# Kernel optimization log

Hardware: AMD Instinct MI355X
Metric: run time of the kernel (lower is better)

## Reference

```python
import jax, jax.numpy as jnp
import numpy as np
import math

D_MODEL = 1024
NUM_HEADS = 16
BATCH = 2
SEQ = 2048

def setup_inputs() -> dict:
    key = jax.random.key(0)
    ks = jax.random.split(key, 9)
    s = 1.0 / math.sqrt(D_MODEL)
    inp = {
        "X": jax.random.normal(ks[0], (BATCH, SEQ, D_MODEL), dtype=jnp.float32),
        "Wq": jax.random.uniform(ks[1], (D_MODEL, D_MODEL), jnp.float32, -s, s),
        "bq": jax.random.uniform(ks[2], (D_MODEL,), jnp.float32, -s, s),
        "Wk": jax.random.uniform(ks[3], (D_MODEL, D_MODEL), jnp.float32, -s, s),
        "bk": jax.random.uniform(ks[4], (D_MODEL,), jnp.float32, -s, s),
        "Wv": jax.random.uniform(ks[5], (D_MODEL, D_MODEL), jnp.float32, -s, s),
        "bv": jax.random.uniform(ks[6], (D_MODEL,), jnp.float32, -s, s),
        "Wo": jax.random.uniform(ks[7], (D_MODEL, D_MODEL), jnp.float32, -s, s),
        "bo": jax.random.uniform(ks[8], (D_MODEL,), jnp.float32, -s, s),
    }
    return inp

def reference(X, Wq, bq, Wk, bk, Wv, bv, Wo, bo):
    B, S, D = X.shape
    H = NUM_HEADS
    dk = D // H
    # QKV projections (Linear: x @ W.T + b; here W stored as [in, out] so x @ W + b)
    q = X @ Wq + bq
    k = X @ Wk + bk
    v = X @ Wv + bv
    # split heads -> [B, H, S, dk]
    q = q.reshape(B, S, H, dk).transpose(0, 2, 1, 3)
    k = k.reshape(B, S, H, dk).transpose(0, 2, 1, 3)
    v = v.reshape(B, S, H, dk).transpose(0, 2, 1, 3)
    scores = jnp.einsum("bhqd,bhkd->bhqk", q, k) / math.sqrt(dk)
    weights = jax.nn.softmax(scores, axis=-1)
    attn = jnp.einsum("bhqk,bhkd->bhqd", weights, v)
    concat = attn.transpose(0, 2, 1, 3).reshape(B, S, D)
    return concat @ Wo + bo
```

## Files before the change

kernel.cpp:

```cpp
#include <hip/hip_runtime.h>
#include <stdint.h>

#define D_MODEL 1024
#define NH      16
#define DKH     64
#define BATCH   2
#define SEQ     2048
#define M_TOK   (BATCH*SEQ)

typedef __attribute__((ext_vector_type(8))) short bf16x8;
typedef __attribute__((ext_vector_type(4))) float f32x4;

__device__ __forceinline__ uint16_t f2b(float f) {
  uint32_t u = __builtin_bit_cast(uint32_t, f);
  return (uint16_t)((u + 0x7FFFu + ((u >> 16) & 1u)) >> 16);
}

__device__ __forceinline__ void gl2lds16(const uint16_t* g, uint16_t* l) {
  __builtin_amdgcn_global_load_lds(
      (const __attribute__((address_space(1))) void*)g,
      (__attribute__((address_space(3))) void*)l, 16, 0, 0);
}

__global__ void convx(const float* __restrict__ X, uint16_t* __restrict__ Xb) {
  int i = (blockIdx.x * 256 + threadIdx.x) * 8;
  float4 a = *(const float4*)(X + i);
  float4 b = *(const float4*)(X + i + 4);
  uint16_t tmp[8] = {f2b(a.x), f2b(a.y), f2b(a.z), f2b(a.w),
                     f2b(b.x), f2b(b.y), f2b(b.z), f2b(b.w)};
  *(uint4*)(Xb + i) = *(const uint4*)tmp;
}

__global__ void wtrans(const float* __restrict__ W0, const float* __restrict__ W1,
                       const float* __restrict__ W2, const float* __restrict__ W3,
                       uint16_t* __restrict__ T0, uint16_t* __restrict__ T1,
                       uint16_t* __restrict__ T2, uint16_t* __restrict__ T3) {
  __shared__ float tile[32][33];
  int z = blockIdx.z;
  const float* W = (z == 0) ? W0 : (z == 1) ? W1 : (z == 2) ? W2 : W3;
  uint16_t*    T = (z == 0) ? T0 : (z == 1) ? T1 : (z == 2) ? T2 : T3;
  int k0 = blockIdx.x * 32, n0 = blockIdx.y * 32;
  int tx = threadIdx.x, ty = threadIdx.y;
  tile[ty][tx] = W[(size_t)(k0 + ty) * D_MODEL + n0 + tx];
  __syncthreads();
  T[(size_t)(n0 + ty) * D_MODEL + k0 + tx] = f2b(tile[tx][ty]);
}

template <bool SWAP>
__device__ __forceinline__ void gemm_core(const uint16_t* __restrict__ A,
                                          const uint16_t* __restrict__ BT,
                                          uint16_t* As, uint16_t* Bs,
                                          int m0, int n0, int kBeg, int kEnd,
                                          f32x4 (&acc)[4][4]) {
  const int t    = threadIdx.x;
  const int lane = t & 63;
  const int qi   = lane & 15, g = lane >> 4;
  const int wm   = (t >> 7) & 1;
  const int wn   = (t >> 6) & 1;
  const int srow = t >> 2;
  const int sc   = (t & 3) ^ ((t >> 3) & 3);
  const int wbase = t & 192;
  const int rch  = (g ^ ((qi >> 1) & 3)) * 8;

  const uint16_t* Ag = A  + (size_t)(m0 + srow) * D_MODEL + sc * 8;
  const uint16_t* Bg = BT + (size_t)(n0 + srow) * D_MODEL + sc * 8;

#pragma unroll
  for (int j = 0; j < 2; j++) {
    gl2lds16(Ag + (size_t)j * 64 * D_MODEL + kBeg, As + (j * 256 + wbase) * 8);
    gl2lds16(Bg + (size_t)j * 64 * D_MODEL + kBeg, Bs + (j * 256 + wbase) * 8);
  }

  int cur = 0;
  for (int k0 = kBeg; k0 < kEnd; k0 += 32) {
    __syncthreads();
    int kn = k0 + 32;
    if (kn < kEnd) {
      int nb = (cur ^ 1) * 4096;
#pragma unroll
      for (int j = 0; j < 2; j++) {
        gl2lds16(Ag + (size_t)j * 64 * D_MODEL + kn, As + nb + (j * 256 + wbase) * 8);
        gl2lds16(Bg + (size_t)j * 64 * D_MODEL + kn, Bs + nb + (j * 256 + wbase) * 8);
      }
    }
    const uint16_t* Ab = As + cur * 4096;
    const uint16_t* Bb = Bs + cur * 4096;
    bf16x8 af[4], bf[4];
#pragma unroll
    for (int i = 0; i < 4; i++) {
      af[i] = *(const bf16x8*)(Ab + (wm * 64 + i * 16 + qi) * 32 + rch);
      bf[i] = *(const bf16x8*)(Bb + (wn * 64 + i * 16 + qi) * 32 + rch);
    }
#pragma unroll
    for (int i = 0; i < 4; i++)
#pragma unroll
      for (int j = 0; j < 4; j++)
        acc[i][j] = SWAP
          ? __builtin_amdgcn_mfma_f32_16x16x32_bf16(bf[j], af[i], acc[i][j], 0, 0, 0)
          : __builtin_amdgcn_mfma_f32_16x16x32_bf16(af[i], bf[j], acc[i][j], 0, 0, 0);
    cur ^= 1;
  }
}

__global__ __launch_bounds__(256) void qkv_gemm(
    const uint16_t* __restrict__ Xb,
    const uint16_t* __restrict__ WqT, const uint16_t* __restrict__ WkT,
    const uint16_t* __restrict__ WvT,
    const float* __restrict__ bq, const float* __restrict__ bk,
    const float* __restrict__ bv,
    uint16_t* __restrict__ Qo, uint16_t* __restrict__ Ko, uint16_t* __restrict__ Vt) {
  __shared__ __align__(16) uint16_t smem[17408];
  uint16_t* As = smem;
  uint16_t* Bs = smem + 8192;
  uint16_t* T  = smem;
  const int z = blockIdx.z;
  const uint16_t* BT  = (z == 0) ? WqT : (z == 1) ? WkT : WvT;
  const float*   bias = (z == 0) ? bq  : (z == 1) ? bk  : bv;
  const int m0 = blockIdx.y * 128, n0 = blockIdx.x * 128;
  const int lane = threadIdx.x & 63, qi = lane & 15, g = lane >> 4;
  const int wm = (threadIdx.x >> 7) & 1, wn = (threadIdx.x >> 6) & 1;
  const float l2e = 1.4426950408889634f * 0.125f;

  const f32x4 ZERO = {0.f, 0.f, 0.f, 0.f};
  f32x4 acc[4][4];
#pragma unroll
  for (int i = 0; i < 4; i++)
#pragma unroll
    for (int j = 0; j < 4; j++) acc[i][j] = ZERO;

  if (z == 2) {
    gemm_core<false>(Xb, BT, As, Bs, m0, n0, 0, D_MODEL, acc);
    __syncthreads();
#pragma unroll
    for (int i = 0; i < 4; i++) {
      int tok = wm * 64 + i * 16 + g * 4;
#pragma unroll
      for (int j = 0; j < 4; j++) {
        int ch = wn * 64 + j * 16 + qi;
        float bb = bias[n0 + ch];
        uint32_t lo = (uint32_t)f2b(acc[i][j][0] + bb) | ((uint32_t)f2b(acc[i][j][1] + bb) << 16);
        uint32_t hi = (uint32_t)f2b(acc[i][j][2] + bb) | ((uint32_t)f2b(acc[i][j][3] + bb) << 16);
        uint2 pk = {lo, hi};
        *(uint2*)(T + ch * 136 + tok) = pk;
      }
    }
    __syncthreads();
    {
      int ch = threadIdx.x >> 1, sh = threadIdx.x & 1;
      const uint16_t* src = T + ch * 136 + sh * 64;
      int bidx = m0 >> 11;
      uint16_t* dst = Vt + ((size_t)(bidx * D_MODEL + n0 + ch)) * SEQ + (m0 & 2047) + sh * 64;
#pragma unroll
      for (int u = 0; u < 8; u++)
        *(uint4*)(dst + u * 8) = *(const uint4*)(src + u * 8);
    }
  } else {
    gemm_core<true>(Xb, BT, As, Bs, m0, n0, 0, D_MODEL, acc);
    uint16_t* O = z ? Ko : Qo;
    const float osc = (z == 0) ? l2e : 1.0f;
#pragma unroll
    for (int i = 0; i < 4; i++) {
      size_t tok = m0 + wm * 64 + i * 16 + qi;
#pragma unroll
      for (int j = 0; j < 4; j++) {
        int ch = n0 + wn * 64 + j * 16 + g * 4;
        float4 bb = *(const float4*)(bias + ch);
        uint32_t lo = (uint32_t)f2b((acc[i][j][0] + bb.x) * osc) |
                      ((uint32_t)f2b((acc[i][j][1] + bb.y) * osc) << 16);
        uint32_t hi = (uint32_t)f2b((acc[i][j][2] + bb.z) * osc) |
                      ((uint32_t)f2b((acc[i][j][3] + bb.w) * osc) << 16);
        uint2 pk = {lo, hi};
        *(uint2*)(O + tok * D_MODEL + ch) = pk;
      }
    }
  }
}

__global__ __launch_bounds__(256) void oproj_gemm(
    const uint16_t* __restrict__ Ab, const uint16_t* __restrict__ WoT,
    const float* __restrict__ bo, float* __restrict__ out) {
  __shared__ __align__(16) uint16_t As[8192];
  __shared__ __align__(16) uint16_t Bs[4096];
  const int t = threadIdx.x;
  const int lane = t & 63, qi = lane & 15, g = lane >> 4;
  const int wm = (t >> 7) & 1;
  const int wn = (t >> 6) & 1;
  const int srow = t >> 2;
  const int sc = (t & 3) ^ ((t >> 3) & 3);
  const int wbase = t & 192;
  const int rch = (g ^ ((qi >> 1) & 3)) * 8;
  const int m0 = blockIdx.y * 128, n0 = blockIdx.x * 64;

  const uint16_t* Ag = Ab  + (size_t)(m0 + srow) * D_MODEL + sc * 8;
  const uint16_t* Bg = WoT + (size_t)(n0 + srow) * D_MODEL + sc * 8;

  const f32x4 ZERO = {0.f, 0.f, 0.f, 0.f};
  f32x4 acc[4][2];
#pragma unroll
  for (int i = 0; i < 4; i++)
#pragma unroll
    for (int j = 0; j < 2; j++) acc[i][j] = ZERO;

  gl2lds16(Ag, As + wbase * 8);
  gl2lds16(Ag + (size_t)64 * D_MODEL, As + (256 + wbase) * 8);
  gl2lds16(Bg, Bs + wbase * 8);

  int cur = 0;
  for (int k0 = 0; k0 < D_MODEL; k0 += 32) {
    __syncthreads();
    int kn = k0 + 32;
    if (kn < D_MODEL) {
      int nbA = (cur ^ 1) * 4096, nbB = (cur ^ 1) * 2048;
      gl2lds16(Ag + kn, As + nbA + wbase * 8);
      gl2lds16(Ag + (size_t)64 * D_MODEL + kn, As + nbA + (256 + wbase) * 8);
      gl2lds16(Bg + kn, Bs + nbB + wbase * 8);
    }
    const uint16_t* Abuf = As + cur * 4096;
    const uint16_t* Bbuf = Bs + cur * 2048;
    bf16x8 af[4], bf[2];
#pragma unroll
    for (int i = 0; i < 4; i++)
      af[i] = *(const bf16x8*)(Abuf + (wm * 64 + i * 16 + qi) * 32 + rch);
#pragma unroll
    for (int j = 0; j < 2; j++)
      bf[j] = *(const bf16x8*)(Bbuf + (wn * 32 + j * 16 + qi) * 32 + rch);
#pragma unroll
    for (int i = 0; i < 4; i++)
#pragma unroll
      for (int j = 0; j < 2; j++)
        acc[i][j] = __builtin_amdgcn_mfma_f32_16x16x32_bf16(bf[j], af[i], acc[i][j], 0, 0, 0);
    cur ^= 1;
  }

#pragma unroll
  for (int i = 0; i < 4; i++) {
    size_t tok = m0 + wm * 64 + i * 16 + qi;
#pragma unroll
    for (int j = 0; j < 2; j++) {
      int ch = n0 + wn * 32 + j * 16 + g * 4;
      float4 bb = *(const float4*)(bo + ch);
      float4 o = {acc[i][j][0] + bb.x, acc[i][j][1] + bb.y,
                  acc[i][j][2] + bb.z, acc[i][j][3] + bb.w};
      *(float4*)(out + tok * D_MODEL + ch) = o;
    }
  }
}

__global__ __launch_bounds__(256) void attn_fwd(
    const uint16_t* __restrict__ Q, const uint16_t* __restrict__ K,
    const uint16_t* __restrict__ Vt, uint16_t* __restrict__ O) {
  __shared__ __align__(16) uint16_t sm[24576];
  uint16_t* Ps = sm + 16384;

  const int t = threadIdx.x, lane = t & 63, w = t >> 6;
  const int g = lane >> 4, qi = lane & 15;
  const int wbase = t & 192;
  const int sc = (t & 3) ^ ((t >> 3) & 3);
  const int rch = (g ^ ((qi >> 1) & 3)) * 8;
  const int key = qi & 7;
  const int q0 = blockIdx.x * 128;
  const int bh = blockIdx.y, b = bh >> 4, h = bh & 15;
  const uint16_t* Qp = Q + (size_t)b * SEQ * D_MODEL + h * DKH;
  const uint16_t* Kp = K + (size_t)b * SEQ * D_MODEL + h * DKH;
  const uint16_t* Vp = Vt + (size_t)bh * DKH * SEQ;

  const int srow = t >> 2, c8 = sc * 8;

#pragma unroll
  for (int hs = 0; hs < 2; hs++)
#pragma unroll
    for (int j = 0; j < 2; j++)
      gl2lds16(Qp + (size_t)(q0 + j * 64 + srow) * D_MODEL + hs * 32 + c8,
               sm + 16384 + hs * 4096 + (j * 256 + wbase) * 8);
  {
    const uint16_t* Kr = Kp + (size_t)srow * D_MODEL;
    const uint16_t* Vr = Vp + (size_t)srow * SEQ;
    gl2lds16(Kr + c8,      sm + wbase * 8);
    gl2lds16(Kr + 32 + c8, sm + 2048 + wbase * 8);
    gl2lds16(Vr + c8,      sm + 8192 + wbase * 8);
    gl2lds16(Vr + 32 + c8, sm + 8192 + 2048 + wbase * 8);
  }
  __syncthreads();

  bf16x8 qf[2][2];
#pragma unroll
  for (int ks = 0; ks < 2; ks++)
#pragma unroll
    for (int i = 0; i < 2; i++)
      qf[ks][i] = *(const bf16x8*)(sm + 16384 + ks * 4096 + (w * 32 + i * 16 + qi) * 32 + rch);
  __syncthreads();

  float lsum[2] = {0.f, 0.f};
  const f32x4 ZERO = {0.f, 0.f, 0.f, 0.f};
  f32x4 oaccT[4][2];
#pragma unroll
  for (int d = 0; d < 4; d++)
#pragma unroll
    for (int i = 0; i < 2; i++) oaccT[d][i] = ZERO;

  int cur = 0;
  for (int kt = 0; kt < SEQ / 64; kt++) {
    if (kt + 1 < SEQ / 64) {
      int nb = (cur ^ 1) * 4096;
      const uint16_t* Kr = Kp + (size_t)((kt + 1) * 64 + srow) * D_MODEL;
      const uint16_t* Vr = Vp + (size_t)srow * SEQ + (kt + 1) * 64;
      gl2lds16(Kr + c8,      sm + nb + wbase * 8);
      gl2lds16(Kr + 32 + c8, sm + nb + 2048 + wbase * 8);
      gl2lds16(Vr + c8,      sm + 8192 + nb + wbase * 8);
      gl2lds16(Vr + 32 + c8, sm + 8192 + nb + 2048 + wbase * 8);
    }
    const uint16_t* Kb = sm + cur * 4096;
    const uint16_t* Vb = sm + 8192 + cur * 4096;

    f32x4 sacc[4][2];
#pragma unroll
    for (int j = 0; j < 4; j++)
#pragma unroll
      for (int i = 0; i < 2; i++) sacc[j][i] = ZERO;
#pragma unroll
    for (int ks = 0; ks < 2; ks++) {
      const uint16_t* Ksb = Kb + ks * 2048;
      bf16x8 kf[4];
#pragma unroll
      for (int j = 0; j < 4; j++)
        kf[j] = *(const bf16x8*)(Ksb + (j * 16 + qi) * 32 + rch);
#pragma unroll
      for (int j = 0; j < 4; j++)
#pragma unroll
        for (int i = 0; i < 2; i++)
          sacc[j][i] = __builtin_amdgcn_mfma_f32_16x16x32_bf16(kf[j], qf[ks][i], sacc[j][i], 0, 0, 0);
    }

#pragma unroll
    for (int i = 0; i < 2; i++) {
      uint16_t* Pr = Ps + (w * 32 + i * 16 + qi) * 64;
#pragma unroll
      for (int j = 0; j < 4; j++) {
        float p0 = __builtin_amdgcn_exp2f(sacc[j][i][0]);
        float p1 = __builtin_amdgcn_exp2f(sacc[j][i][1]);
        float p2 = __builtin_amdgcn_exp2f(sacc[j][i][2]);
        float p3 = __builtin_amdgcn_exp2f(sacc[j][i][3]);
        lsum[i] += (p0 + p1) + (p2 + p3);
        uint2 pk = {__builtin_amdgcn_perm(__builtin_bit_cast(uint32_t, p1),
                                          __builtin_bit_cast(uint32_t, p0), 0x07060302u),
                    __builtin_amdgcn_perm(__builtin_bit_cast(uint32_t, p3),
                                          __builtin_bit_cast(uint32_t, p2), 0x07060302u)};
        *(uint2*)(Pr + (((j * 4 + g) ^ (2 * key)) << 2)) = pk;
      }
    }

#pragma unroll
    for (int ks = 0; ks < 2; ks++) {
      const uint16_t* Vsb = Vb + ks * 2048;
      bf16x8 vf[4], pf[2];
#pragma unroll
      for (int d = 0; d < 4; d++)
        vf[d] = *(const bf16x8*)(Vsb + (d * 16 + qi) * 32 + rch);
#pragma unroll
      for (int i = 0; i < 2; i++)
        pf[i] = *(const bf16x8*)(Ps + (w * 32 + i * 16 + qi) * 64 +
                                 (((ks * 4 + g) ^ key) << 3));
#pragma unroll
      for (int d = 0; d < 4; d++)
#pragma unroll
        for (int i = 0; i < 2; i++)
          oaccT[d][i] = __builtin_amdgcn_mfma_f32_16x16x32_bf16(vf[d], pf[i], oaccT[d][i], 0, 0, 0);
    }

    if (kt + 1 < SEQ / 64) __syncthreads();
    cur ^= 1;
  }

#pragma unroll
  for (int i = 0; i < 2; i++) {
    lsum[i] += __shfl_xor(lsum[i], 16, 64);
    lsum[i] += __shfl_xor(lsum[i], 32, 64);
  }
  float rl[2] = {1.f / lsum[0], 1.f / lsum[1]};

#pragma unroll
  for (int i = 0; i < 2; i++) {
    size_t row = (size_t)b * SEQ + q0 + w * 32 + i * 16 + qi;
#pragma unroll
    for (int d = 0; d < 4; d++) {
      uint32_t lo = (uint32_t)f2b(oaccT[d][i][0] * rl[i]) |
                    ((uint32_t)f2b(oaccT[d][i][1] * rl[i]) << 16);
      uint32_t hi = (uint32_t)f2b(oaccT[d][i][2] * rl[i]) |
                    ((uint32_t)f2b(oaccT[d][i][3] * rl[i]) << 16);
      uint2 pk = {lo, hi};
      *(uint2*)(O + row * D_MODEL + h * DKH + d * 16 + g * 4) = pk;
    }
  }
}

extern "C" void kernel_launch(void* const* d_in, const int* in_sizes, int n_in,
                              void* d_out, int out_size, void* d_ws, size_t ws_size,
                              hipStream_t stream) {
  (void)in_sizes; (void)n_in; (void)out_size; (void)ws_size;
  const float* X  = (const float*)d_in[0];
  const float* Wq = (const float*)d_in[1];
  const float* bq = (const float*)d_in[2];
  const float* Wk = (const float*)d_in[3];
  const float* bk = (const float*)d_in[4];
  const float* Wv = (const float*)d_in[5];
  const float* bv = (const float*)d_in[6];
  const float* Wo = (const float*)d_in[7];
  const float* bo = (const float*)d_in[8];
  float* out = (float*)d_out;

  char* p = (char*)d_ws;
  uint16_t* Xb  = (uint16_t*)p; p += (size_t)M_TOK * D_MODEL * 2;
  uint16_t* WqT = (uint16_t*)p; p += (size_t)D_MODEL * D_MODEL * 2;
  uint16_t* WkT = (uint16_t*)p; p += (size_t)D_MODEL * D_MODEL * 2;
  uint16_t* WvT = (uint16_t*)p; p += (size_t)D_MODEL * D_MODEL * 2;
  uint16_t* WoT = (uint16_t*)p; p += (size_t)D_MODEL * D_MODEL * 2;
  uint16_t* Qw  = (uint16_t*)p; p += (size_t)M_TOK * D_MODEL * 2;
  uint16_t* Kw  = (uint16_t*)p; p += (size_t)M_TOK * D_MODEL * 2;
  uint16_t* Vt  = (uint16_t*)p; p += (size_t)M_TOK * D_MODEL * 2;
  uint16_t* Ob  = (uint16_t*)p; p += (size_t)M_TOK * D_MODEL * 2;

  convx<<<(M_TOK * D_MODEL) / (256 * 8), 256, 0, stream>>>(X, Xb);
  wtrans<<<dim3(32, 32, 4), dim3(32, 32), 0, stream>>>(Wq, Wk, Wv, Wo, WqT, WkT, WvT, WoT);
  qkv_gemm<<<dim3(8, 32, 3), 256, 0, stream>>>(Xb, WqT, WkT, WvT, bq, bk, bv, Qw, Kw, Vt);
  attn_fwd<<<dim3(SEQ / 128, BATCH * NH), 256, 0, stream>>>(Qw, Kw, Vt, Ob);
  oproj_gemm<<<dim3(16, 32), 256, 0, stream>>>(Ob, WoT, bo, out);
}
```

Baseline: 203.9 us.

## Split attention block across 8 waves with 16 query rows each

The attention kernel moves from 256 to 512 threads per block, so each wave handles 16 query rows instead of 32. Q fragments are now loaded straight from global memory into registers rather than staged through LDS, and the K/V tile loads are divided across the two 256-thread halves. s_setprio raises wave priority around the MFMA groups. The aim is more waves in flight to hide latency and lower per-wave register pressure. The cost is that each wave now issues K/V fragment LDS reads for half as many MFMAs, so LDS traffic per unit of compute doubles.

```diff
diff --git a/kernel.cpp b/kernel.cpp
--- a/kernel.cpp
+++ b/kernel.cpp
@@ -246,7 +246,7 @@
   }
 }
 
-__global__ __launch_bounds__(256) void attn_fwd(
+__global__ __launch_bounds__(512, 4) void attn_fwd(
     const uint16_t* __restrict__ Q, const uint16_t* __restrict__ K,
     const uint16_t* __restrict__ Vt, uint16_t* __restrict__ O) {
   __shared__ __align__(16) uint16_t sm[24576];
@@ -254,8 +254,6 @@
 
   const int t = threadIdx.x, lane = t & 63, w = t >> 6;
   const int g = lane >> 4, qi = lane & 15;
-  const int wbase = t & 192;
-  const int sc = (t & 3) ^ ((t >> 3) & 3);
   const int rch = (g ^ ((qi >> 1) & 3)) * 8;
   const int key = qi & 7;
   const int q0 = blockIdx.x * 128;
@@ -264,59 +262,45 @@
   const uint16_t* Kp = K + (size_t)b * SEQ * D_MODEL + h * DKH;
   const uint16_t* Vp = Vt + (size_t)bh * DKH * SEQ;
 
-  const int srow = t >> 2, c8 = sc * 8;
-
-#pragma unroll
-  for (int hs = 0; hs < 2; hs++)
-#pragma unroll
-    for (int j = 0; j < 2; j++)
-      gl2lds16(Qp + (size_t)(q0 + j * 64 + srow) * D_MODEL + hs * 32 + c8,
-               sm + 16384 + hs * 4096 + (j * 256 + wbase) * 8);
+  const int tt = t & 255, hs = t >> 8;
+  const int srow = tt >> 2;
+  const int sc = (tt & 3) ^ ((tt >> 3) & 3);
+  const int wbase = tt & 192;
+
+  bf16x8 qf[2];
   {
-    const uint16_t* Kr = Kp + (size_t)srow * D_MODEL;
-    const uint16_t* Vr = Vp + (size_t)srow * SEQ;
-    gl2lds16(Kr + c8,      sm + wbase * 8);
-    gl2lds16(Kr + 32 + c8, sm + 2048 + wbase * 8);
-    gl2lds16(Vr + c8,      sm + 8192 + wbase * 8);
-    gl2lds16(Vr + 32 + c8, sm + 8192 + 2048 + wbase * 8);
-  }
+    const uint16_t* Qr = Qp + (size_t)(q0 + w * 16 + qi) * D_MODEL + g * 8;
+    qf[0] = *(const bf16x8*)(Qr);
+    qf[1] = *(const bf16x8*)(Qr + 32);
+  }
+
+  gl2lds16(Kp + (size_t)srow * D_MODEL + hs * 32 + sc * 8,
+           sm + hs * 2048 + wbase * 8);
+  gl2lds16(Vp + (size_t)srow * SEQ + hs * 32 + sc * 8,
+           sm + 8192 + hs * 2048 + wbase * 8);
   __syncthreads();
 
-  bf16x8 qf[2][2];
-#pragma unroll
-  for (int ks = 0; ks < 2; ks++)
-#pragma unroll
-    for (int i = 0; i < 2; i++)
-      qf[ks][i] = *(const bf16x8*)(sm + 16384 + ks * 4096 + (w * 32 + i * 16 + qi) * 32 + rch);
-  __syncthreads();
-
-  float lsum[2] = {0.f, 0.f};
+  float lsum = 0.f;
   const f32x4 ZERO = {0.f, 0.f, 0.f, 0.f};
-  f32x4 oaccT[4][2];
-#pragma unroll
-  for (int d = 0; d < 4; d++)
-#pragma unroll
-    for (int i = 0; i < 2; i++) oaccT[d][i] = ZERO;
+  f32x4 oaccT[4];
+#pragma unroll
+  for (int d = 0; d < 4; d++) oaccT[d] = ZERO;
 
   int cur = 0;
   for (int kt = 0; kt < SEQ / 64; kt++) {
     if (kt + 1 < SEQ / 64) {
       int nb = (cur ^ 1) * 4096;
-      const uint16_t* Kr = Kp + (size_t)((kt + 1) * 64 + srow) * D_MODEL;
-      const uint16_t* Vr = Vp + (size_t)srow * SEQ + (kt + 1) * 64;
-      gl2lds16(Kr + c8,      sm + nb + wbase * 8);
-      gl2lds16(Kr + 32 + c8, sm + nb + 2048 + wbase * 8);
-      gl2lds16(Vr + c8,      sm + 8192 + nb + wbase * 8);
-      gl2lds16(Vr + 32 + c8, sm + 8192 + nb + 2048 + wbase * 8);
+      gl2lds16(Kp + (size_t)((kt + 1) * 64 + srow) * D_MODEL + hs * 32 + sc * 8,
+               sm + nb + hs * 2048 + wbase * 8);
+      gl2lds16(Vp + (size_t)srow * SEQ + (kt + 1) * 64 + hs * 32 + sc * 8,
+               sm + 8192 + nb + hs * 2048 + wbase * 8);
     }
     const uint16_t* Kb = sm + cur * 4096;
     const uint16_t* Vb = sm + 8192 + cur * 4096;
 
-    f32x4 sacc[4][2];
-#pragma unroll
-    for (int j = 0; j < 4; j++)
-#pragma unroll
-      for (int i = 0; i < 2; i++) sacc[j][i] = ZERO;
+    f32x4 sacc[4];
+#pragma unroll
+    for (int j = 0; j < 4; j++) sacc[j] = ZERO;
 #pragma unroll
     for (int ks = 0; ks < 2; ks++) {
       const uint16_t* Ksb = Kb + ks * 2048;
@@ -324,69 +308,59 @@
 #pragma unroll
       for (int j = 0; j < 4; j++)
         kf[j] = *(const bf16x8*)(Ksb + (j * 16 + qi) * 32 + rch);
+      __builtin_amdgcn_s_setprio(1);
 #pragma unroll
       for (int j = 0; j < 4; j++)
-#pragma unroll
-        for (int i = 0; i < 2; i++)
-          sacc[j][i] = __builtin_amdgcn_mfma_f32_16x16x32_bf16(kf[j], qf[ks][i], sacc[j][i], 0, 0, 0);
-    }
-
-#pragma unroll
-    for (int i = 0; i < 2; i++) {
-      uint16_t* Pr = Ps + (w * 32 + i * 16 + qi) * 64;
-#pragma unroll
-      for (int j = 0; j < 4; j++) {
-        float p0 = __builtin_amdgcn_exp2f(sacc[j][i][0]);
-        float p1 = __builtin_amdgcn_exp2f(sacc[j][i][1]);
-        float p2 = __builtin_amdgcn_exp2f(sacc[j][i][2]);
-        float p3 = __builtin_amdgcn_exp2f(sacc[j][i][3]);
-        lsum[i] += (p0 + p1) + (p2 + p3);
-        uint2 pk = {__builtin_amdgcn_perm(__builtin_bit_cast(uint32_t, p1),
-                                          __builtin_bit_cast(uint32_t, p0), 0x07060302u),
-                    __builtin_amdgcn_perm(__builtin_bit_cast(uint32_t, p3),
-                                          __builtin_bit_cast(uint32_t, p2), 0x07060302u)};
-        *(uint2*)(Pr + (((j * 4 + g) ^ (2 * key)) << 2)) = pk;
-      }
+        sacc[j] = __builtin_amdgcn_mfma_f32_16x16x32_bf16(kf[j], qf[ks], sacc[j], 0, 0, 0);
+      __builtin_amdgcn_s_setprio(0);
+    }
+
+    uint16_t* Pr = Ps + (w * 16 + qi) * 64;
+#pragma unroll
+    for (int j = 0; j < 4; j++) {
+      float p0 = __builtin_amdgcn_exp2f(sacc[j][0]);
+      float p1 = __builtin_amdgcn_exp2f(sacc[j][1]);
+      float p2 = __builtin_amdgcn_exp2f(sacc[j][2]);
+      float p3 = __builtin_amdgcn_exp2f(sacc[j][3]);
+      lsum += (p0 + p1) + (p2 + p3);
+      uint2 pk = {__builtin_amdgcn_perm(__builtin_bit_cast(uint32_t, p1),
+                                        __builtin_bit_cast(uint32_t, p0), 0x07060302u),
+                  __builtin_amdgcn_perm(__builtin_bit_cast(uint32_t, p3),
+                                        __builtin_bit_cast(uint32_t, p2), 0x07060302u)};
+      *(uint2*)(Pr + (((j * 4 + g) ^ (2 * key)) << 2)) = pk;
     }
 
 #pragma unroll
     for (int ks = 0; ks < 2; ks++) {
       const uint16_t* Vsb = Vb + ks * 2048;
-      bf16x8 vf[4], pf[2];
+      bf16x8 vf[4];
 #pragma unroll
       for (int d = 0; d < 4; d++)
         vf[d] = *(const bf16x8*)(Vsb + (d * 16 + qi) * 32 + rch);
-#pragma unroll
-      for (int i = 0; i < 2; i++)
-        pf[i] = *(const bf16x8*)(Ps + (w * 32 + i * 16 + qi) * 64 +
-                                 (((ks * 4 + g) ^ key) << 3));
+      bf16x8 pf = *(const bf16x8*)(Pr + (((ks * 4 + g) ^ key) << 3));
+      __builtin_amdgcn_s_setprio(1);
 #pragma unroll
       for (int d = 0; d < 4; d++)
-#pragma unroll
-        for (int i = 0; i < 2; i++)
-          oaccT[d][i] = __builtin_amdgcn_mfma_f32_16x16x32_bf16(vf[d], pf[i], oaccT[d][i], 0, 0, 0);
+        oaccT[d] = __builtin_amdgcn_mfma_f32_16x16x32_bf16(vf[d], pf, oaccT[d], 0, 0, 0);
+      __builtin_amdgcn_s_setprio(0);
     }
 
     if (kt + 1 < SEQ / 64) __syncthreads();
     cur ^= 1;
   }
 
-#pragma unroll
-  for (int i = 0; i < 2; i++) {
-    lsum[i] += __shfl_xor(lsum[i], 16, 64);
-    lsum[i] += __shfl_xor(lsum[i], 32, 64);
-  }
-  float rl[2] = {1.f / lsum[0], 1.f / lsum[1]};
-
-#pragma unroll
-  for (int i = 0; i < 2; i++) {
-    size_t row = (size_t)b * SEQ + q0 + w * 32 + i * 16 + qi;
+  lsum += __shfl_xor(lsum, 16, 64);
+  lsum += __shfl_xor(lsum, 32, 64);
+  float rl = 1.f / lsum;
+
+  {
+    size_t row = (size_t)b * SEQ + q0 + w * 16 + qi;
 #pragma unroll
     for (int d = 0; d < 4; d++) {
-      uint32_t lo = (uint32_t)f2b(oaccT[d][i][0] * rl[i]) |
-                    ((uint32_t)f2b(oaccT[d][i][1] * rl[i]) << 16);
-      uint32_t hi = (uint32_t)f2b(oaccT[d][i][2] * rl[i]) |
-                    ((uint32_t)f2b(oaccT[d][i][3] * rl[i]) << 16);
+      uint32_t lo = (uint32_t)f2b(oaccT[d][0] * rl) |
+                    ((uint32_t)f2b(oaccT[d][1] * rl) << 16);
+      uint32_t hi = (uint32_t)f2b(oaccT[d][2] * rl) |
+                    ((uint32_t)f2b(oaccT[d][3] * rl) << 16);
       uint2 pk = {lo, hi};
       *(uint2*)(O + row * D_MODEL + h * DKH + d * 16 + g * 4) = pk;
     }
@@ -422,6 +396,6 @@
   convx<<<(M_TOK * D_MODEL) / (256 * 8), 256, 0, stream>>>(X, Xb);
   wtrans<<<dim3(32, 32, 4), dim3(32, 32), 0, stream>>>(Wq, Wk, Wv, Wo, WqT, WkT, WvT, WoT);
   qkv_gemm<<<dim3(8, 32, 3), 256, 0, stream>>>(Xb, WqT, WkT, WvT, bq, bk, bv, Qw, Kw, Vt);
-  attn_fwd<<<dim3(SEQ / 128, BATCH * NH), 256, 0, stream>>>(Qw, Kw, Vt, Ob);
+  attn_fwd<<<dim3(SEQ / 128, BATCH * NH), 512, 0, stream>>>(Qw, Kw, Vt, Ob);
   oproj_gemm<<<dim3(16, 32), 256, 0, stream>>>(Ob, WoT, bo, out);
 }
```

Result: no change. 199.9 us (-1.9%).

## Enlarge attention block to 256 queries with 8 waves sharing K/V tiles

Applied to the files above, without the earlier changes.

Doubles the attention work-group to 512 threads covering 256 query rows, so each K/V tile staged in LDS is reused by eight waves instead of four. This halves the global K/V loads per query. Q fragments are now loaded straight from global memory into registers instead of going through LDS. MFMA sections are wrapped in s_setprio to favour matrix issue. The trade-offs are a larger LDS footprint, half as many blocks, and coarser scheduling across CUs.

```diff
diff --git a/kernel.cpp b/kernel.cpp
--- a/kernel.cpp
+++ b/kernel.cpp
@@ -246,48 +246,39 @@
   }
 }
 
-__global__ __launch_bounds__(256) void attn_fwd(
+__global__ __launch_bounds__(512, 2) void attn_fwd(
     const uint16_t* __restrict__ Q, const uint16_t* __restrict__ K,
     const uint16_t* __restrict__ Vt, uint16_t* __restrict__ O) {
-  __shared__ __align__(16) uint16_t sm[24576];
+  __shared__ __align__(16) uint16_t sm[32768];
   uint16_t* Ps = sm + 16384;
 
   const int t = threadIdx.x, lane = t & 63, w = t >> 6;
   const int g = lane >> 4, qi = lane & 15;
-  const int wbase = t & 192;
-  const int sc = (t & 3) ^ ((t >> 3) & 3);
   const int rch = (g ^ ((qi >> 1) & 3)) * 8;
   const int key = qi & 7;
-  const int q0 = blockIdx.x * 128;
+  const int q0 = blockIdx.x * 256;
   const int bh = blockIdx.y, b = bh >> 4, h = bh & 15;
   const uint16_t* Qp = Q + (size_t)b * SEQ * D_MODEL + h * DKH;
   const uint16_t* Kp = K + (size_t)b * SEQ * D_MODEL + h * DKH;
   const uint16_t* Vp = Vt + (size_t)bh * DKH * SEQ;
 
-  const int srow = t >> 2, c8 = sc * 8;
-
-#pragma unroll
-  for (int hs = 0; hs < 2; hs++)
-#pragma unroll
-    for (int j = 0; j < 2; j++)
-      gl2lds16(Qp + (size_t)(q0 + j * 64 + srow) * D_MODEL + hs * 32 + c8,
-               sm + 16384 + hs * 4096 + (j * 256 + wbase) * 8);
-  {
-    const uint16_t* Kr = Kp + (size_t)srow * D_MODEL;
-    const uint16_t* Vr = Vp + (size_t)srow * SEQ;
-    gl2lds16(Kr + c8,      sm + wbase * 8);
-    gl2lds16(Kr + 32 + c8, sm + 2048 + wbase * 8);
-    gl2lds16(Vr + c8,      sm + 8192 + wbase * 8);
-    gl2lds16(Vr + 32 + c8, sm + 8192 + 2048 + wbase * 8);
-  }
-  __syncthreads();
+  const int tt = t & 255, hs = t >> 8;
+  const int srow = tt >> 2;
+  const int sc = (tt & 3) ^ ((tt >> 3) & 3);
+  const int wbase = tt & 192;
 
   bf16x8 qf[2][2];
 #pragma unroll
-  for (int ks = 0; ks < 2; ks++)
-#pragma unroll
-    for (int i = 0; i < 2; i++)
-      qf[ks][i] = *(const bf16x8*)(sm + 16384 + ks * 4096 + (w * 32 + i * 16 + qi) * 32 + rch);
+  for (int i = 0; i < 2; i++) {
+    const uint16_t* Qr = Qp + (size_t)(q0 + w * 32 + i * 16 + qi) * D_MODEL + g * 8;
+    qf[0][i] = *(const bf16x8*)(Qr);
+    qf[1][i] = *(const bf16x8*)(Qr + 32);
+  }
+
+  gl2lds16(Kp + (size_t)srow * D_MODEL + hs * 32 + sc * 8,
+           sm + hs * 2048 + wbase * 8);
+  gl2lds16(Vp + (size_t)srow * SEQ + hs * 32 + sc * 8,
+           sm + 8192 + hs * 2048 + wbase * 8);
   __syncthreads();
 
   float lsum[2] = {0.f, 0.f};
@@ -302,12 +293,10 @@
   for (int kt = 0; kt < SEQ / 64; kt++) {
     if (kt + 1 < SEQ / 64) {
       int nb = (cur ^ 1) * 4096;
-      const uint16_t* Kr = Kp + (size_t)((kt + 1) * 64 + srow) * D_MODEL;
-      const uint16_t* Vr = Vp + (size_t)srow * SEQ + (kt + 1) * 64;
-      gl2lds16(Kr + c8,      sm + nb + wbase * 8);
-      gl2lds16(Kr + 32 + c8, sm + nb + 2048 + wbase * 8);
-      gl2lds16(Vr + c8,      sm + 8192 + nb + wbase * 8);
-      gl2lds16(Vr + 32 + c8, sm + 8192 + nb + 2048 + wbase * 8);
+      gl2lds16(Kp + (size_t)((kt + 1) * 64 + srow) * D_MODEL + hs * 32 + sc * 8,
+               sm + nb + hs * 2048 + wbase * 8);
+      gl2lds16(Vp + (size_t)srow * SEQ + (kt + 1) * 64 + hs * 32 + sc * 8,
+               sm + 8192 + nb + hs * 2048 + wbase * 8);
     }
     const uint16_t* Kb = sm + cur * 4096;
     const uint16_t* Vb = sm + 8192 + cur * 4096;
@@ -324,11 +313,13 @@
 #pragma unroll
       for (int j = 0; j < 4; j++)
         kf[j] = *(const bf16x8*)(Ksb + (j * 16 + qi) * 32 + rch);
+      __builtin_amdgcn_s_setprio(1);
 #pragma unroll
       for (int j = 0; j < 4; j++)
 #pragma unroll
         for (int i = 0; i < 2; i++)
           sacc[j][i] = __builtin_amdgcn_mfma_f32_16x16x32_bf16(kf[j], qf[ks][i], sacc[j][i], 0, 0, 0);
+      __builtin_amdgcn_s_setprio(0);
     }
 
 #pragma unroll
@@ -360,11 +351,13 @@
       for (int i = 0; i < 2; i++)
         pf[i] = *(const bf16x8*)(Ps + (w * 32 + i * 16 + qi) * 64 +
                                  (((ks * 4 + g) ^ key) << 3));
+      __builtin_amdgcn_s_setprio(1);
 #pragma unroll
       for (int d = 0; d < 4; d++)
 #pragma unroll
         for (int i = 0; i < 2; i++)
           oaccT[d][i] = __builtin_amdgcn_mfma_f32_16x16x32_bf16(vf[d], pf[i], oaccT[d][i], 0, 0, 0);
+      __builtin_amdgcn_s_setprio(0);
     }
 
     if (kt + 1 < SEQ / 64) __syncthreads();
@@ -422,6 +415,6 @@
   convx<<<(M_TOK * D_MODEL) / (256 * 8), 256, 0, stream>>>(X, Xb);
   wtrans<<<dim3(32, 32, 4), dim3(32, 32), 0, stream>>>(Wq, Wk, Wv, Wo, WqT, WkT, WvT, WoT);
   qkv_gemm<<<dim3(8, 32, 3), 256, 0, stream>>>(Xb, WqT, WkT, WvT, bq, bk, bv, Qw, Kw, Vt);
-  attn_fwd<<<dim3(SEQ / 128, BATCH * NH), 256, 0, stream>>>(Qw, Kw, Vt, Ob);
+  attn_fwd<<<dim3(SEQ / 256, BATCH * NH), 512, 0, stream>>>(Qw, Kw, Vt, Ob);
   oproj_gemm<<<dim3(16, 32), 256, 0, stream>>>(Ob, WoT, bo, out);
 }
```

New measurement: 194.6 us. 1.05x faster.

## Load Q fragments directly to registers, reorder attention grid, add MFMA priority hints

Applied to the files above, without the earlier changes.

Q fragments now come straight from global memory into registers instead of being staged through LDS, which removes one barrier and the LDS round trip. The attention grid is transposed so blocks for different heads launch next to each other, changing L2 reuse of K/V across blocks. launch_bounds gains a minimum of 2 blocks per CU, and s_setprio brackets the MFMA sections so waves doing matrix math get issue priority. The direct Q load uses uncoalesced 16-byte strided reads, and the occupancy bound may limit registers.

```diff
diff --git a/kernel.cpp b/kernel.cpp
--- a/kernel.cpp
+++ b/kernel.cpp
@@ -246,7 +246,7 @@
   }
 }
 
-__global__ __launch_bounds__(256) void attn_fwd(
+__global__ __launch_bounds__(256, 2) void attn_fwd(
     const uint16_t* __restrict__ Q, const uint16_t* __restrict__ K,
     const uint16_t* __restrict__ Vt, uint16_t* __restrict__ O) {
   __shared__ __align__(16) uint16_t sm[24576];
@@ -254,24 +254,27 @@
 
   const int t = threadIdx.x, lane = t & 63, w = t >> 6;
   const int g = lane >> 4, qi = lane & 15;
-  const int wbase = t & 192;
-  const int sc = (t & 3) ^ ((t >> 3) & 3);
   const int rch = (g ^ ((qi >> 1) & 3)) * 8;
   const int key = qi & 7;
-  const int q0 = blockIdx.x * 128;
-  const int bh = blockIdx.y, b = bh >> 4, h = bh & 15;
+  const int q0 = blockIdx.y * 128;
+  const int bh = blockIdx.x, b = bh >> 4, h = bh & 15;
   const uint16_t* Qp = Q + (size_t)b * SEQ * D_MODEL + h * DKH;
   const uint16_t* Kp = K + (size_t)b * SEQ * D_MODEL + h * DKH;
   const uint16_t* Vp = Vt + (size_t)bh * DKH * SEQ;
 
-  const int srow = t >> 2, c8 = sc * 8;
-
-#pragma unroll
-  for (int hs = 0; hs < 2; hs++)
-#pragma unroll
-    for (int j = 0; j < 2; j++)
-      gl2lds16(Qp + (size_t)(q0 + j * 64 + srow) * D_MODEL + hs * 32 + c8,
-               sm + 16384 + hs * 4096 + (j * 256 + wbase) * 8);
+  const int srow = t >> 2;
+  const int sc = (t & 3) ^ ((t >> 3) & 3);
+  const int wbase = t & 192;
+  const int c8 = sc * 8;
+
+  bf16x8 qf[2][2];
+#pragma unroll
+  for (int i = 0; i < 2; i++) {
+    const uint16_t* Qr = Qp + (size_t)(q0 + w * 32 + i * 16 + qi) * D_MODEL + g * 8;
+    qf[0][i] = *(const bf16x8*)(Qr);
+    qf[1][i] = *(const bf16x8*)(Qr + 32);
+  }
+
   {
     const uint16_t* Kr = Kp + (size_t)srow * D_MODEL;
     const uint16_t* Vr = Vp + (size_t)srow * SEQ;
@@ -280,14 +283,6 @@
     gl2lds16(Vr + c8,      sm + 8192 + wbase * 8);
     gl2lds16(Vr + 32 + c8, sm + 8192 + 2048 + wbase * 8);
   }
-  __syncthreads();
-
-  bf16x8 qf[2][2];
-#pragma unroll
-  for (int ks = 0; ks < 2; ks++)
-#pragma unroll
-    for (int i = 0; i < 2; i++)
-      qf[ks][i] = *(const bf16x8*)(sm + 16384 + ks * 4096 + (w * 32 + i * 16 + qi) * 32 + rch);
   __syncthreads();
 
   float lsum[2] = {0.f, 0.f};
@@ -324,11 +319,13 @@
 #pragma unroll
       for (int j = 0; j < 4; j++)
         kf[j] = *(const bf16x8*)(Ksb + (j * 16 + qi) * 32 + rch);
+      __builtin_amdgcn_s_setprio(1);
 #pragma unroll
       for (int j = 0; j < 4; j++)
 #pragma unroll
         for (int i = 0; i < 2; i++)
           sacc[j][i] = __builtin_amdgcn_mfma_f32_16x16x32_bf16(kf[j], qf[ks][i], sacc[j][i], 0, 0, 0);
+      __builtin_amdgcn_s_setprio(0);
     }
 
 #pragma unroll
@@ -360,11 +357,13 @@
       for (int i = 0; i < 2; i++)
         pf[i] = *(const bf16x8*)(Ps + (w * 32 + i * 16 + qi) * 64 +
                                  (((ks * 4 + g) ^ key) << 3));
+      __builtin_amdgcn_s_setprio(1);
 #pragma unroll
       for (int d = 0; d < 4; d++)
 #pragma unroll
         for (int i = 0; i < 2; i++)
           oaccT[d][i] = __builtin_amdgcn_mfma_f32_16x16x32_bf16(vf[d], pf[i], oaccT[d][i], 0, 0, 0);
+      __builtin_amdgcn_s_setprio(0);
     }
 
     if (kt + 1 < SEQ / 64) __syncthreads();
@@ -422,6 +421,6 @@
   convx<<<(M_TOK * D_MODEL) / (256 * 8), 256, 0, stream>>>(X, Xb);
   wtrans<<<dim3(32, 32, 4), dim3(32, 32), 0, stream>>>(Wq, Wk, Wv, Wo, WqT, WkT, WvT, WoT);
   qkv_gemm<<<dim3(8, 32, 3), 256, 0, stream>>>(Xb, WqT, WkT, WvT, bq, bk, bv, Qw, Kw, Vt);
-  attn_fwd<<<dim3(SEQ / 128, BATCH * NH), 256, 0, stream>>>(Qw, Kw, Vt, Ob);
+  attn_fwd<<<dim3(BATCH * NH, SEQ / 128), 256, 0, stream>>>(Qw, Kw, Vt, Ob);
   oproj_gemm<<<dim3(16, 32), 256, 0, stream>>>(Ob, WoT, bo, out);
 }
```

After: 198.1 us. -2.8%, faster.
